# Optimization experiments

Hardware: AMD Instinct MI355X
Metric: run time of the kernel (lower is better)

## Reference

```python
import jax, jax.numpy as jnp
import numpy as np

EPS = 1e-5
NH, NP = 4, 4  # num_heads, num_points (num_levels = 1)


def layer_norm(x, g, b):
    m = jnp.mean(x, -1, keepdims=True)
    xc = x - m
    v = jnp.mean(xc * xc, -1, keepdims=True)
    return xc * jax.lax.rsqrt(v + EPS) * g + b


def setup_inputs() -> dict:
    key = jax.random.key(0)
    ks = jax.random.split(key, 8)
    B, C, H, W = 8, 256, 64, 64
    s = 0.02
    return {
        "x1": jax.random.normal(ks[0], (B, C, H, W), jnp.float32),
        "x2": jax.random.normal(ks[1], (B, C, H, W), jnp.float32),
        "ln1_g": jnp.ones((C,), jnp.float32),
        "ln1_b": jnp.zeros((C,), jnp.float32),
        "ln2_g": jnp.ones((C,), jnp.float32),
        "ln2_b": jnp.zeros((C,), jnp.float32),
        "pos_scale": jnp.ones((1,), jnp.float32),
        "W_off": jax.random.normal(ks[2], (C, NH * NP * 2), jnp.float32) * s,
        "b_off": jax.random.normal(ks[3], (NH * NP * 2,), jnp.float32) * 0.5,
        "W_att": jax.random.normal(ks[4], (C, NH * NP), jnp.float32) * s,
        "b_att": jnp.zeros((NH * NP,), jnp.float32),
        "W_val": jax.random.normal(ks[5], (C, C), jnp.float32) * s,
        "b_val": jnp.zeros((C,), jnp.float32),
        "W_out": jax.random.normal(ks[6], (C, C), jnp.float32) * s,
        "b_out": jnp.zeros((C,), jnp.float32),
    }


def reference(x1, x2, ln1_g, ln1_b, ln2_g, ln2_b, pos_scale,
              W_off, b_off, W_att, b_att, W_val, b_val, W_out, b_out):
    B, C, H, W = x1.shape
    Nq = H * W
    d = C // NH
    q_in = x1.reshape(B, C, Nq).transpose(0, 2, 1)   # (B, Nq, C)
    v_in = x2.reshape(B, C, Nq).transpose(0, 2, 1)   # (B, Nv, C), identity

    # ScaledSinuEmbedding positional encoding over the query sequence
    inv_freq = 1.0 / (10000.0 ** (jnp.arange(0, C, 2, dtype=jnp.float32) / C))
    sinu = jnp.arange(Nq, dtype=jnp.float32)[:, None] * inv_freq[None, :]
    qpos = jnp.concatenate([jnp.sin(sinu), jnp.cos(sinu)], -1) * pos_scale  # (Nq, C)

    query = layer_norm(q_in, ln1_g, ln1_b) + qpos[None]
    value = layer_norm(v_in, ln2_g, ln2_b) @ W_val + b_val                 # (B, Nv, C)
    value = value.reshape(B, Nq, NH, d).transpose(0, 2, 1, 3)              # (B, NH, Nv, d)

    off = (query @ W_off + b_off).reshape(B, Nq, NH, NP, 2)
    att = jax.nn.softmax((query @ W_att + b_att).reshape(B, Nq, NH, NP), axis=-1)

    # reference points: normalized pixel centers of the query grid
    ry, rx = jnp.meshgrid((jnp.arange(H, dtype=jnp.float32) + 0.5) / H,
                          (jnp.arange(W, dtype=jnp.float32) + 0.5) / W,
                          indexing="ij")
    ref = jnp.stack([rx.ravel(), ry.ravel()], -1)                          # (Nq, 2) as (x, y)

    norm = jnp.array([W, H], jnp.float32)  # offset_normalizer = (W, H)
    loc = ref[None, :, None, None, :] + off / norm                         # (B,Nq,NH,NP,2)
    loc = loc.transpose(0, 2, 1, 3, 4)                                     # (B,NH,Nq,NP,2)
    # grid_sample(align_corners=False): pixel = normalized * size - 0.5
    px = loc[..., 0] * W - 0.5
    py = loc[..., 1] * H - 0.5
    x0 = jnp.floor(px); y0 = jnp.floor(py)
    wx = px - x0; wy = py - y0
    x0i = x0.astype(jnp.int32); y0i = y0.astype(jnp.int32)

    def gather(ix, iy):
        # zero padding for out-of-bounds corners, like grid_sample(padding_mode='zeros')
        valid = ((ix >= 0) & (ix < W) & (iy >= 0) & (iy < H)).astype(value.dtype)
        idx = jnp.clip(iy, 0, H - 1) * W + jnp.clip(ix, 0, W - 1)          # (B,NH,Nq,NP)
        g = jnp.take_along_axis(value, idx.reshape(B, NH, Nq * NP, 1), axis=2)
        return g.reshape(B, NH, Nq, NP, d) * valid[..., None]

    sampled = (gather(x0i, y0i) * ((1 - wx) * (1 - wy))[..., None]
               + gather(x0i + 1, y0i) * (wx * (1 - wy))[..., None]
               + gather(x0i, y0i + 1) * ((1 - wx) * wy)[..., None]
               + gather(x0i + 1, y0i + 1) * (wx * wy)[..., None])          # (B,NH,Nq,NP,d)

    out = jnp.sum(sampled * att.transpose(0, 2, 1, 3)[..., None], axis=3)  # (B,NH,Nq,d)
    out = out.transpose(0, 2, 1, 3).reshape(B, Nq, C)
    out = out @ W_out + b_out + v_in                                       # + identity (x2)
    return out.transpose(0, 2, 1).reshape(B, C, H, W)
```

## Files before the change

kernel.cpp:

```cpp
#include <hip/hip_runtime.h>
#include <math.h>

namespace {
constexpr int kC = 256;
constexpr int kNq = 4096;
constexpr int kM = 32768;
}

typedef __attribute__((ext_vector_type(8))) short short8;
typedef __attribute__((ext_vector_type(4))) float f32x4;

__device__ inline unsigned short f2bf(float f) {
  union { float f; unsigned u; } v; v.f = f;
  unsigned r = (v.u + 0x7FFFu + ((v.u >> 16) & 1u)) >> 16;
  return (unsigned short)r;
}
__device__ inline float uasf(unsigned u) {
  union { unsigned u; float f; } v; v.u = u; return v.f;
}

__global__ __launch_bounds__(256)
void prep_weights_kernel(const float* __restrict__ Wv, const float* __restrict__ Wo,
                         const float* __restrict__ Woff, const float* __restrict__ Watt,
                         unsigned short* __restrict__ WvT, unsigned short* __restrict__ WoT,
                         unsigned short* __restrict__ WoaT) {
  const int i = blockIdx.x * 256 + threadIdx.x;
  {
    const int n = i >> 8, k = i & 255;
    WvT[i] = f2bf(Wv[k * 256 + n]);
    WoT[i] = f2bf(Wo[k * 256 + n]);
  }
  if (i < 16384) {
    const int j = i >> 8, k = i & 255;
    float v = 0.f;
    if (j < 32) v = Woff[k * 32 + j];
    else if (j < 48) v = Watt[k * 16 + (j - 32)];
    WoaT[i] = f2bf(v);
  }
}


__global__ __launch_bounds__(256)
void fused_val_kernel(const float* __restrict__ X, const float* __restrict__ gam,
                      const float* __restrict__ beta, const unsigned short* __restrict__ Wt,
                      const float* __restrict__ bias, unsigned short* __restrict__ V) {
  __shared__ unsigned short As[64][264];
  __shared__ float scratch[256][33];
  __shared__ float psum[8][32];
  __shared__ float psq[8][32];
  __shared__ float smean[64];
  __shared__ float srstd[64];

  const int m0 = blockIdx.x * 64;
  const int b = m0 >> 12;
  const int n0 = m0 & 4095;
  const int tid = threadIdx.x;
  const float gc = gam[tid];
  const float bc = beta[tid];
  const float* Xb = X + (size_t)b * kC * kNq;

  for (int grp = 0; grp < 2; ++grp) {
    float4 vbuf[8];
#pragma unroll
    for (int it = 0; it < 8; ++it) {
      const int i = it * 256 + tid;
      const int c = i >> 3, q4 = (i & 7) * 4;
      vbuf[it] = *(const float4*)&Xb[(size_t)c * kNq + n0 + grp * 32 + q4];
    }
#pragma unroll
    for (int it = 0; it < 8; ++it) {
      const int i = it * 256 + tid;
      const int c = i >> 3, q4 = (i & 7) * 4;
      scratch[c][q4 + 0] = vbuf[it].x;
      scratch[c][q4 + 1] = vbuf[it].y;
      scratch[c][q4 + 2] = vbuf[it].z;
      scratch[c][q4 + 3] = vbuf[it].w;
    }
    __syncthreads();
    {
      const int nn = tid & 31, cg = tid >> 5;
      float s = 0.f, sq = 0.f;
#pragma unroll
      for (int cc = 0; cc < 32; ++cc) {
        const float v = scratch[cg * 32 + cc][nn];
        s += v; sq += v * v;
      }
      psum[cg][nn] = s; psq[cg][nn] = sq;
    }
    __syncthreads();
    if (tid < 32) {
      float S = 0.f, Q = 0.f;
#pragma unroll
      for (int g = 0; g < 8; ++g) { S += psum[g][tid]; Q += psq[g][tid]; }
      const float m = S * (1.f / 256.f);
      const float v = Q * (1.f / 256.f) - m * m;
      smean[grp * 32 + tid] = m;
      srstd[grp * 32 + tid] = rsqrtf(v + 1e-5f);
    }
    __syncthreads();
    for (int q = 0; q < 32; ++q) {
      const int row = grp * 32 + q;
      As[row][tid] = f2bf((scratch[tid][q] - smean[row]) * srstd[row] * gc + bc);
    }
    __syncthreads();
  }

  const int lane = tid & 63, w = tid >> 6;
  const int l15 = lane & 15, quad = lane >> 4;
  f32x4 acc[4][4];
#pragma unroll
  for (int i = 0; i < 4; ++i)
#pragma unroll
    for (int j = 0; j < 4; ++j) acc[i][j] = (f32x4){0.f, 0.f, 0.f, 0.f};

#pragma unroll
  for (int s = 0; s < 8; ++s) {
    short8 af[4], wf[4];
#pragma unroll
    for (int t = 0; t < 4; ++t) af[t] = *(const short8*)&As[t * 16 + l15][s * 32 + quad * 8];
#pragma unroll
    for (int t = 0; t < 4; ++t)
      wf[t] = *(const short8*)&Wt[(size_t)(w * 64 + t * 16 + l15) * 256 + s * 32 + quad * 8];
#pragma unroll
    for (int i = 0; i < 4; ++i)
#pragma unroll
      for (int j = 0; j < 4; ++j)
        acc[i][j] = __builtin_amdgcn_mfma_f32_16x16x32_bf16(af[i], wf[j], acc[i][j], 0, 0, 0);
  }
#pragma unroll
  for (int i = 0; i < 4; ++i)
#pragma unroll
    for (int j = 0; j < 4; ++j) {
      const int n = w * 64 + j * 16 + l15;
      const float bn = bias[n];
#pragma unroll
      for (int r = 0; r < 4; ++r) {
        const int m = m0 + i * 16 + quad * 4 + r;
        V[(size_t)m * 256 + n] = f2bf(acc[i][j][r] + bn);
      }
    }
}

__global__ __launch_bounds__(256)
void fused_offatt_kernel(const float* __restrict__ X, const float* __restrict__ gam,
                         const float* __restrict__ beta, const float* __restrict__ ps,
                         const unsigned short* __restrict__ Wt,
                         const float* __restrict__ boff, const float* __restrict__ batt,
                         float* __restrict__ RAW) {
  __shared__ unsigned short As[64][264];
  __shared__ float scratch[256][33];
  __shared__ float psum[8][32];
  __shared__ float psq[8][32];
  __shared__ float smean[64];
  __shared__ float srstd[64];

  const int m0 = blockIdx.x * 64;
  const int b = m0 >> 12;
  const int n0 = m0 & 4095;
  const int tid = threadIdx.x;
  const float gc = gam[tid];
  const float bc = beta[tid];
  const float scale = ps[0];
  const int i2 = (tid < 128) ? tid : (tid - 128);
  const float invf = powf(10000.f, -(float)(2 * i2) * (1.f / 256.f));
  const float* Xb = X + (size_t)b * kC * kNq;

  for (int grp = 0; grp < 2; ++grp) {
    float4 vbuf[8];
#pragma unroll
    for (int it = 0; it < 8; ++it) {
      const int i = it * 256 + tid;
      const int c = i >> 3, q4 = (i & 7) * 4;
      vbuf[it] = *(const float4*)&Xb[(size_t)c * kNq + n0 + grp * 32 + q4];
    }
#pragma unroll
    for (int it = 0; it < 8; ++it) {
      const int i = it * 256 + tid;
      const int c = i >> 3, q4 = (i & 7) * 4;
      scratch[c][q4 + 0] = vbuf[it].x;
      scratch[c][q4 + 1] = vbuf[it].y;
      scratch[c][q4 + 2] = vbuf[it].z;
      scratch[c][q4 + 3] = vbuf[it].w;
    }
    __syncthreads();
    {
      const int nn = tid & 31, cg = tid >> 5;
      float s = 0.f, sq = 0.f;
#pragma unroll
      for (int cc = 0; cc < 32; ++cc) {
        const float v = scratch[cg * 32 + cc][nn];
        s += v; sq += v * v;
      }
      psum[cg][nn] = s; psq[cg][nn] = sq;
    }
    __syncthreads();
    if (tid < 32) {
      float S = 0.f, Q = 0.f;
#pragma unroll
      for (int g = 0; g < 8; ++g) { S += psum[g][tid]; Q += psq[g][tid]; }
      const float m = S * (1.f / 256.f);
      const float v = Q * (1.f / 256.f) - m * m;
      smean[grp * 32 + tid] = m;
      srstd[grp * 32 + tid] = rsqrtf(v + 1e-5f);
    }
    __syncthreads();
    for (int q = 0; q < 32; ++q) {
      const int row = grp * 32 + q;
      float val = (scratch[tid][q] - smean[row]) * srstd[row] * gc + bc;
      const float a = (float)(n0 + row) * invf;
      val += ((tid < 128) ? sinf(a) : cosf(a)) * scale;
      As[row][tid] = f2bf(val);
    }
    __syncthreads();
  }

  const int lane = tid & 63, w = tid >> 6;
  const int l15 = lane & 15, quad = lane >> 4;
  f32x4 acc[3];
#pragma unroll
  for (int j = 0; j < 3; ++j) acc[j] = (f32x4){0.f, 0.f, 0.f, 0.f};
#pragma unroll
  for (int s = 0; s < 8; ++s) {
    short8 af = *(const short8*)&As[w * 16 + l15][s * 32 + quad * 8];
    short8 wf[3];
#pragma unroll
    for (int t = 0; t < 3; ++t)
      wf[t] = *(const short8*)&Wt[(size_t)(t * 16 + l15) * 256 + s * 32 + quad * 8];
#pragma unroll
    for (int j = 0; j < 3; ++j)
      acc[j] = __builtin_amdgcn_mfma_f32_16x16x32_bf16(af, wf[j], acc[j], 0, 0, 0);
  }
#pragma unroll
  for (int j = 0; j < 3; ++j) {
    const int n = j * 16 + l15;
    const float bn = (n < 32) ? boff[n] : batt[n - 32];
#pragma unroll
    for (int r = 0; r < 4; ++r) {
      const int m = m0 + w * 16 + quad * 4 + r;
      RAW[(size_t)m * 48 + n] = acc[j][r] + bn;
    }
  }
}

__global__ __launch_bounds__(256)
void sample_kernel(const float* __restrict__ RAW, const unsigned short* __restrict__ V,
                   unsigned short* __restrict__ AO) {
  __shared__ int sidx[128][4];
  __shared__ float swgt[128][4];
  const int blk = blockIdx.x;
  const int m0 = ((blk & 7) * 512 + (blk >> 3)) * 8;
  const int b = m0 >> 12;
  const int tid = threadIdx.x;

  if (tid < 128) {
    const int q_l = tid >> 4, h = (tid >> 2) & 3, p = tid & 3;
    const int m = m0 + q_l;
    const float* raw = RAW + (size_t)m * 48;
    const float l0 = raw[32 + h * 4 + 0];
    const float l1 = raw[32 + h * 4 + 1];
    const float l2 = raw[32 + h * 4 + 2];
    const float l3 = raw[32 + h * 4 + 3];
    const float mx = fmaxf(fmaxf(l0, l1), fmaxf(l2, l3));
    const float e0 = expf(l0 - mx), e1 = expf(l1 - mx), e2 = expf(l2 - mx), e3 = expf(l3 - mx);
    const float lp = (p == 0) ? e0 : (p == 1) ? e1 : (p == 2) ? e2 : e3;
    const float attp = lp / (e0 + e1 + e2 + e3);

    const float ox = raw[h * 8 + p * 2 + 0];
    const float oy = raw[h * 8 + p * 2 + 1];
    const float px = (float)(m & 63) + ox;
    const float py = (float)((m >> 6) & 63) + oy;
    const float fx = floorf(px), fy = floorf(py);
    const float wx = px - fx, wy = py - fy;
    const int x0 = (int)fx, y0 = (int)fy;
#pragma unroll
    for (int c = 0; c < 4; ++c) {
      const int dx = c & 1, dy = c >> 1;
      const int xx = x0 + dx, yy = y0 + dy;
      const bool valid = (xx >= 0) & (xx < 64) & (yy >= 0) & (yy < 64);
      const float wc = (dx ? wx : 1.f - wx) * (dy ? wy : 1.f - wy) * attp;
      swgt[tid][c] = valid ? wc : 0.f;
      const int xc = min(max(xx, 0), 63), yc = min(max(yy, 0), 63);
      sidx[tid][c] = yc * 64 + xc;
    }
  }
  __syncthreads();

  const int q_l = tid >> 5, sub = tid & 31;
  const int h = sub >> 3, c8 = (sub & 7) * 8;
  const int trip0 = q_l * 16 + h * 4;
  const unsigned short* vb = V + (size_t)b * kNq * kC + h * 64 + c8;
  float acc[8] = {};
#pragma unroll
  for (int p = 0; p < 4; ++p) {
    const int4 idx = *(const int4*)&sidx[trip0 + p][0];
    const float4 wv = *(const float4*)&swgt[trip0 + p][0];
    const int ia[4] = {idx.x, idx.y, idx.z, idx.w};
    const float wa[4] = {wv.x, wv.y, wv.z, wv.w};
#pragma unroll
    for (int c = 0; c < 4; ++c) {
      const uint4 u = *(const uint4*)&vb[(size_t)ia[c] * kC];
      const float w = wa[c];
      acc[0] = fmaf(w, uasf(u.x << 16), acc[0]);
      acc[1] = fmaf(w, uasf(u.x & 0xffff0000u), acc[1]);
      acc[2] = fmaf(w, uasf(u.y << 16), acc[2]);
      acc[3] = fmaf(w, uasf(u.y & 0xffff0000u), acc[3]);
      acc[4] = fmaf(w, uasf(u.z << 16), acc[4]);
      acc[5] = fmaf(w, uasf(u.z & 0xffff0000u), acc[5]);
      acc[6] = fmaf(w, uasf(u.w << 16), acc[6]);
      acc[7] = fmaf(w, uasf(u.w & 0xffff0000u), acc[7]);
    }
  }
  const int m = m0 + q_l;
  short8 outv;
#pragma unroll
  for (int e = 0; e < 8; ++e) outv[e] = (short)f2bf(acc[e]);
  *(short8*)&AO[(size_t)m * kC + h * 64 + c8] = outv;
}

__global__ __launch_bounds__(256, 3)
void gemm_out_kernel(const unsigned short* __restrict__ Wt,
                     const unsigned short* __restrict__ AO,
                     const float* __restrict__ bias, const float* __restrict__ x2,
                     float* __restrict__ OUT) {
  __shared__ unsigned short Bs[64][264];
  const int q0 = blockIdx.x * 64;
  const int tid = threadIdx.x;
  const int lane = tid & 63, w = tid >> 6;
  const int l15 = lane & 15, quad = lane >> 4;

#pragma unroll
  for (int it = 0; it < 8; ++it) {
    const int i = it * 256 + tid;
    const int r = i >> 5, cc = (i & 31) * 8;
    *(short8*)&Bs[r][cc] = *(const short8*)&AO[(size_t)(q0 + r) * 256 + cc];
  }
  __syncthreads();

  f32x4 acc[4][4];
#pragma unroll
  for (int i = 0; i < 4; ++i)
#pragma unroll
    for (int j = 0; j < 4; ++j) acc[i][j] = (f32x4){0.f, 0.f, 0.f, 0.f};

#pragma unroll
  for (int s = 0; s < 8; ++s) {
    short8 wf[4], bf[4];
#pragma unroll
    for (int t = 0; t < 4; ++t)
      wf[t] = *(const short8*)&Wt[(size_t)(w * 64 + t * 16 + l15) * 256 + s * 32 + quad * 8];
#pragma unroll
    for (int t = 0; t < 4; ++t) bf[t] = *(const short8*)&Bs[t * 16 + l15][s * 32 + quad * 8];
#pragma unroll
    for (int i = 0; i < 4; ++i)
#pragma unroll
      for (int j = 0; j < 4; ++j)
        acc[i][j] = __builtin_amdgcn_mfma_f32_16x16x32_bf16(wf[i], bf[j], acc[i][j], 0, 0, 0);
  }

  const int b = q0 >> 12;
  const int qb = q0 & 4095;
#pragma unroll
  for (int i = 0; i < 4; ++i) {
#pragma unroll
    for (int r = 0; r < 4; ++r) {
      const int c = w * 64 + i * 16 + quad * 4 + r;
      const float bc = bias[c];
      const size_t rowbase = ((size_t)b * 256 + c) * 4096 + qb;
#pragma unroll
      for (int j = 0; j < 4; ++j) {
        const int q = j * 16 + l15;
        OUT[rowbase + q] = acc[i][j][r] + bc + x2[rowbase + q];
      }
    }
  }
}

extern "C" void kernel_launch(void* const* d_in, const int* in_sizes, int n_in,
                              void* d_out, int out_size, void* d_ws, size_t ws_size,
                              hipStream_t stream) {
  const float* x1 = (const float*)d_in[0];
  const float* x2 = (const float*)d_in[1];
  const float* ln1_g = (const float*)d_in[2];
  const float* ln1_b = (const float*)d_in[3];
  const float* ln2_g = (const float*)d_in[4];
  const float* ln2_b = (const float*)d_in[5];
  const float* pos_scale = (const float*)d_in[6];
  const float* W_off = (const float*)d_in[7];
  const float* b_off = (const float*)d_in[8];
  const float* W_att = (const float*)d_in[9];
  const float* b_att = (const float*)d_in[10];
  const float* W_val = (const float*)d_in[11];
  const float* b_val = (const float*)d_in[12];
  const float* W_out = (const float*)d_in[13];
  const float* b_out = (const float*)d_in[14];
  float* out = (float*)d_out;

  char* ws = (char*)d_ws;
  const size_t plane2 = (size_t)kM * kC * sizeof(unsigned short);
  unsigned short* Vb   = (unsigned short*)(ws);
  unsigned short* AOb  = (unsigned short*)(ws + plane2);
  float* RAW           = (float*)(ws + 2 * plane2);
  unsigned short* WvT  = (unsigned short*)(ws + 2 * plane2 + (size_t)kM * 48 * 4);
  unsigned short* WoT  = WvT + 65536;
  unsigned short* WoaT = WoT + 65536;

  prep_weights_kernel<<<256, 256, 0, stream>>>(W_val, W_out, W_off, W_att, WvT, WoT, WoaT);
  fused_offatt_kernel<<<kM / 64, 256, 0, stream>>>(x1, ln1_g, ln1_b, pos_scale, WoaT,
                                                   b_off, b_att, RAW);
  fused_val_kernel<<<kM / 64, 256, 0, stream>>>(x2, ln2_g, ln2_b, WvT, b_val, Vb);
  sample_kernel<<<kM / 8, 256, 0, stream>>>(RAW, Vb, AOb);
  gemm_out_kernel<<<kM / 64, 256, 0, stream>>>(WoT, AOb, b_out, x2, out);
}
```

Baseline: 201.6 us.

## Merge LN-GEMM kernels and fuse sampling with output projection

Result: faster. 185.0 us (-8.2%).

```diff
diff --git a/kernel.cpp b/kernel.cpp
--- a/kernel.cpp
+++ b/kernel.cpp
@@ -39,11 +39,16 @@
   }
 }
 
-
 __global__ __launch_bounds__(256)
-void fused_val_kernel(const float* __restrict__ X, const float* __restrict__ gam,
-                      const float* __restrict__ beta, const unsigned short* __restrict__ Wt,
-                      const float* __restrict__ bias, unsigned short* __restrict__ V) {
+void fused_ln_gemm_kernel(const float* __restrict__ x1, const float* __restrict__ x2,
+                          const float* __restrict__ ln1_g, const float* __restrict__ ln1_b,
+                          const float* __restrict__ ln2_g, const float* __restrict__ ln2_b,
+                          const float* __restrict__ ps,
+                          const unsigned short* __restrict__ WvT,
+                          const float* __restrict__ b_val, unsigned short* __restrict__ V,
+                          const unsigned short* __restrict__ WoaT,
+                          const float* __restrict__ boff, const float* __restrict__ batt,
+                          float* __restrict__ RAW) {
   __shared__ unsigned short As[64][264];
   __shared__ float scratch[256][33];
   __shared__ float psum[8][32];
@@ -51,12 +56,20 @@
   __shared__ float smean[64];
   __shared__ float srstd[64];
 
-  const int m0 = blockIdx.x * 64;
+  const int mode = blockIdx.x & 1;
+  const int m0 = (blockIdx.x >> 1) * 64;
   const int b = m0 >> 12;
   const int n0 = m0 & 4095;
   const int tid = threadIdx.x;
-  const float gc = gam[tid];
-  const float bc = beta[tid];
+  const float* X = mode ? x1 : x2;
+  const float gc = mode ? ln1_g[tid] : ln2_g[tid];
+  const float bc = mode ? ln1_b[tid] : ln2_b[tid];
+  float scale = 0.f, invf = 0.f;
+  if (mode) {
+    scale = ps[0];
+    const int i2 = (tid < 128) ? tid : (tid - 128);
+    invf = powf(10000.f, -(float)(2 * i2) * (1.f / 256.f));
+  }
   const float* Xb = X + (size_t)b * kC * kNq;
 
   for (int grp = 0; grp < 2; ++grp) {
@@ -98,162 +111,107 @@
       srstd[grp * 32 + tid] = rsqrtf(v + 1e-5f);
     }
     __syncthreads();
-    for (int q = 0; q < 32; ++q) {
-      const int row = grp * 32 + q;
-      As[row][tid] = f2bf((scratch[tid][q] - smean[row]) * srstd[row] * gc + bc);
+    if (mode) {
+      for (int q = 0; q < 32; ++q) {
+        const int row = grp * 32 + q;
+        float val = (scratch[tid][q] - smean[row]) * srstd[row] * gc + bc;
+        const float a = (float)(n0 + row) * invf;
+        val += ((tid < 128) ? sinf(a) : cosf(a)) * scale;
+        As[row][tid] = f2bf(val);
+      }
+    } else {
+      for (int q = 0; q < 32; ++q) {
+        const int row = grp * 32 + q;
+        As[row][tid] = f2bf((scratch[tid][q] - smean[row]) * srstd[row] * gc + bc);
+      }
     }
     __syncthreads();
   }
 
   const int lane = tid & 63, w = tid >> 6;
   const int l15 = lane & 15, quad = lane >> 4;
-  f32x4 acc[4][4];
-#pragma unroll
-  for (int i = 0; i < 4; ++i)
-#pragma unroll
-    for (int j = 0; j < 4; ++j) acc[i][j] = (f32x4){0.f, 0.f, 0.f, 0.f};
-
-#pragma unroll
-  for (int s = 0; s < 8; ++s) {
-    short8 af[4], wf[4];
-#pragma unroll
-    for (int t = 0; t < 4; ++t) af[t] = *(const short8*)&As[t * 16 + l15][s * 32 + quad * 8];
-#pragma unroll
-    for (int t = 0; t < 4; ++t)
-      wf[t] = *(const short8*)&Wt[(size_t)(w * 64 + t * 16 + l15) * 256 + s * 32 + quad * 8];
+
+  if (mode == 0) {
+    f32x4 acc[4][4];
 #pragma unroll
     for (int i = 0; i < 4; ++i)
 #pragma unroll
-      for (int j = 0; j < 4; ++j)
-        acc[i][j] = __builtin_amdgcn_mfma_f32_16x16x32_bf16(af[i], wf[j], acc[i][j], 0, 0, 0);
-  }
-#pragma unroll
-  for (int i = 0; i < 4; ++i)
-#pragma unroll
-    for (int j = 0; j < 4; ++j) {
-      const int n = w * 64 + j * 16 + l15;
-      const float bn = bias[n];
+      for (int j = 0; j < 4; ++j) acc[i][j] = (f32x4){0.f, 0.f, 0.f, 0.f};
+#pragma unroll
+    for (int s = 0; s < 8; ++s) {
+      short8 af[4], wf[4];
+#pragma unroll
+      for (int t = 0; t < 4; ++t) af[t] = *(const short8*)&As[t * 16 + l15][s * 32 + quad * 8];
+#pragma unroll
+      for (int t = 0; t < 4; ++t)
+        wf[t] = *(const short8*)&WvT[(size_t)(w * 64 + t * 16 + l15) * 256 + s * 32 + quad * 8];
+#pragma unroll
+      for (int i = 0; i < 4; ++i)
+#pragma unroll
+        for (int j = 0; j < 4; ++j)
+          acc[i][j] = __builtin_amdgcn_mfma_f32_16x16x32_bf16(af[i], wf[j], acc[i][j], 0, 0, 0);
+    }
+#pragma unroll
+    for (int i = 0; i < 4; ++i)
+#pragma unroll
+      for (int j = 0; j < 4; ++j) {
+        const int n = w * 64 + j * 16 + l15;
+        const float bn = b_val[n];
+#pragma unroll
+        for (int r = 0; r < 4; ++r) {
+          const int m = m0 + i * 16 + quad * 4 + r;
+          V[(size_t)m * 256 + n] = f2bf(acc[i][j][r] + bn);
+        }
+      }
+  } else {
+    f32x4 acc[3];
+#pragma unroll
+    for (int j = 0; j < 3; ++j) acc[j] = (f32x4){0.f, 0.f, 0.f, 0.f};
+#pragma unroll
+    for (int s = 0; s < 8; ++s) {
+      short8 af = *(const short8*)&As[w * 16 + l15][s * 32 + quad * 8];
+      short8 wf[3];
+#pragma unroll
+      for (int t = 0; t < 3; ++t)
+        wf[t] = *(const short8*)&WoaT[(size_t)(t * 16 + l15) * 256 + s * 32 + quad * 8];
+#pragma unroll
+      for (int j = 0; j < 3; ++j)
+        acc[j] = __builtin_amdgcn_mfma_f32_16x16x32_bf16(af, wf[j], acc[j], 0, 0, 0);
+    }
+#pragma unroll
+    for (int j = 0; j < 3; ++j) {
+      const int n = j * 16 + l15;
+      const float bn = (n < 32) ? boff[n] : batt[n - 32];
 #pragma unroll
       for (int r = 0; r < 4; ++r) {
-        const int m = m0 + i * 16 + quad * 4 + r;
-        V[(size_t)m * 256 + n] = f2bf(acc[i][j][r] + bn);
-      }
-    }
+        const int m = m0 + w * 16 + quad * 4 + r;
+        RAW[(size_t)m * 48 + n] = acc[j][r] + bn;
+      }
+    }
+  }
 }
 
 __global__ __launch_bounds__(256)
-void fused_offatt_kernel(const float* __restrict__ X, const float* __restrict__ gam,
-                         const float* __restrict__ beta, const float* __restrict__ ps,
-                         const unsigned short* __restrict__ Wt,
-                         const float* __restrict__ boff, const float* __restrict__ batt,
-                         float* __restrict__ RAW) {
-  __shared__ unsigned short As[64][264];
-  __shared__ float scratch[256][33];
-  __shared__ float psum[8][32];
-  __shared__ float psq[8][32];
-  __shared__ float smean[64];
-  __shared__ float srstd[64];
-
-  const int m0 = blockIdx.x * 64;
-  const int b = m0 >> 12;
-  const int n0 = m0 & 4095;
+void sample_out_kernel(const float* __restrict__ RAW, const unsigned short* __restrict__ V,
+                       const unsigned short* __restrict__ Wt,
+                       const float* __restrict__ bias, const float* __restrict__ x2,
+                       float* __restrict__ OUT) {
+  __shared__ unsigned short Bs[64][264];
+  __shared__ __align__(16) char smemA[32768];
+  int (*sidx)[4] = (int(*)[4])smemA;
+  float (*swgt)[4] = (float(*)[4])(smemA + 16384);
+  float* ot = (float*)smemA;
+
+  const int blk = blockIdx.x;
+  const int b = blk & 7;
+  const int tile = blk >> 3;
+  const int m0 = b * 4096 + tile * 64;
   const int tid = threadIdx.x;
-  const float gc = gam[tid];
-  const float bc = beta[tid];
-  const float scale = ps[0];
-  const int i2 = (tid < 128) ? tid : (tid - 128);
-  const float invf = powf(10000.f, -(float)(2 * i2) * (1.f / 256.f));
-  const float* Xb = X + (size_t)b * kC * kNq;
-
-  for (int grp = 0; grp < 2; ++grp) {
-    float4 vbuf[8];
-#pragma unroll
-    for (int it = 0; it < 8; ++it) {
-      const int i = it * 256 + tid;
-      const int c = i >> 3, q4 = (i & 7) * 4;
-      vbuf[it] = *(const float4*)&Xb[(size_t)c * kNq + n0 + grp * 32 + q4];
-    }
-#pragma unroll
-    for (int it = 0; it < 8; ++it) {
-      const int i = it * 256 + tid;
-      const int c = i >> 3, q4 = (i & 7) * 4;
-      scratch[c][q4 + 0] = vbuf[it].x;
-      scratch[c][q4 + 1] = vbuf[it].y;
-      scratch[c][q4 + 2] = vbuf[it].z;
-      scratch[c][q4 + 3] = vbuf[it].w;
-    }
-    __syncthreads();
-    {
-      const int nn = tid & 31, cg = tid >> 5;
-      float s = 0.f, sq = 0.f;
-#pragma unroll
-      for (int cc = 0; cc < 32; ++cc) {
-        const float v = scratch[cg * 32 + cc][nn];
-        s += v; sq += v * v;
-      }
-      psum[cg][nn] = s; psq[cg][nn] = sq;
-    }
-    __syncthreads();
-    if (tid < 32) {
-      float S = 0.f, Q = 0.f;
-#pragma unroll
-      for (int g = 0; g < 8; ++g) { S += psum[g][tid]; Q += psq[g][tid]; }
-      const float m = S * (1.f / 256.f);
-      const float v = Q * (1.f / 256.f) - m * m;
-      smean[grp * 32 + tid] = m;
-      srstd[grp * 32 + tid] = rsqrtf(v + 1e-5f);
-    }
-    __syncthreads();
-    for (int q = 0; q < 32; ++q) {
-      const int row = grp * 32 + q;
-      float val = (scratch[tid][q] - smean[row]) * srstd[row] * gc + bc;
-      const float a = (float)(n0 + row) * invf;
-      val += ((tid < 128) ? sinf(a) : cosf(a)) * scale;
-      As[row][tid] = f2bf(val);
-    }
-    __syncthreads();
-  }
-
-  const int lane = tid & 63, w = tid >> 6;
-  const int l15 = lane & 15, quad = lane >> 4;
-  f32x4 acc[3];
-#pragma unroll
-  for (int j = 0; j < 3; ++j) acc[j] = (f32x4){0.f, 0.f, 0.f, 0.f};
-#pragma unroll
-  for (int s = 0; s < 8; ++s) {
-    short8 af = *(const short8*)&As[w * 16 + l15][s * 32 + quad * 8];
-    short8 wf[3];
-#pragma unroll
-    for (int t = 0; t < 3; ++t)
-      wf[t] = *(const short8*)&Wt[(size_t)(t * 16 + l15) * 256 + s * 32 + quad * 8];
-#pragma unroll
-    for (int j = 0; j < 3; ++j)
-      acc[j] = __builtin_amdgcn_mfma_f32_16x16x32_bf16(af, wf[j], acc[j], 0, 0, 0);
-  }
-#pragma unroll
-  for (int j = 0; j < 3; ++j) {
-    const int n = j * 16 + l15;
-    const float bn = (n < 32) ? boff[n] : batt[n - 32];
-#pragma unroll
-    for (int r = 0; r < 4; ++r) {
-      const int m = m0 + w * 16 + quad * 4 + r;
-      RAW[(size_t)m * 48 + n] = acc[j][r] + bn;
-    }
-  }
-}
-
-__global__ __launch_bounds__(256)
-void sample_kernel(const float* __restrict__ RAW, const unsigned short* __restrict__ V,
-                   unsigned short* __restrict__ AO) {
-  __shared__ int sidx[128][4];
-  __shared__ float swgt[128][4];
-  const int blk = blockIdx.x;
-  const int m0 = ((blk & 7) * 512 + (blk >> 3)) * 8;
-  const int b = m0 >> 12;
-  const int tid = threadIdx.x;
-
-  if (tid < 128) {
-    const int q_l = tid >> 4, h = (tid >> 2) & 3, p = tid & 3;
+
+#pragma unroll
+  for (int t = 0; t < 4; ++t) {
+    const int trip = t * 256 + tid;
+    const int q_l = trip >> 4, h = (trip >> 2) & 3, p = trip & 3;
     const int m = m0 + q_l;
     const float* raw = RAW + (size_t)m * 48;
     const float l0 = raw[32 + h * 4 + 0];
@@ -278,70 +236,55 @@
       const int xx = x0 + dx, yy = y0 + dy;
       const bool valid = (xx >= 0) & (xx < 64) & (yy >= 0) & (yy < 64);
       const float wc = (dx ? wx : 1.f - wx) * (dy ? wy : 1.f - wy) * attp;
-      swgt[tid][c] = valid ? wc : 0.f;
+      swgt[trip][c] = valid ? wc : 0.f;
       const int xc = min(max(xx, 0), 63), yc = min(max(yy, 0), 63);
-      sidx[tid][c] = yc * 64 + xc;
+      sidx[trip][c] = yc * 64 + xc;
     }
   }
   __syncthreads();
 
-  const int q_l = tid >> 5, sub = tid & 31;
-  const int h = sub >> 3, c8 = (sub & 7) * 8;
-  const int trip0 = q_l * 16 + h * 4;
-  const unsigned short* vb = V + (size_t)b * kNq * kC + h * 64 + c8;
-  float acc[8] = {};
-#pragma unroll
-  for (int p = 0; p < 4; ++p) {
-    const int4 idx = *(const int4*)&sidx[trip0 + p][0];
-    const float4 wv = *(const float4*)&swgt[trip0 + p][0];
-    const int ia[4] = {idx.x, idx.y, idx.z, idx.w};
-    const float wa[4] = {wv.x, wv.y, wv.z, wv.w};
-#pragma unroll
-    for (int c = 0; c < 4; ++c) {
-      const uint4 u = *(const uint4*)&vb[(size_t)ia[c] * kC];
-      const float w = wa[c];
-      acc[0] = fmaf(w, uasf(u.x << 16), acc[0]);
-      acc[1] = fmaf(w, uasf(u.x & 0xffff0000u), acc[1]);
-      acc[2] = fmaf(w, uasf(u.y << 16), acc[2]);
-      acc[3] = fmaf(w, uasf(u.y & 0xffff0000u), acc[3]);
-      acc[4] = fmaf(w, uasf(u.z << 16), acc[4]);
-      acc[5] = fmaf(w, uasf(u.z & 0xffff0000u), acc[5]);
-      acc[6] = fmaf(w, uasf(u.w << 16), acc[6]);
-      acc[7] = fmaf(w, uasf(u.w & 0xffff0000u), acc[7]);
-    }
-  }
-  const int m = m0 + q_l;
-  short8 outv;
-#pragma unroll
-  for (int e = 0; e < 8; ++e) outv[e] = (short)f2bf(acc[e]);
-  *(short8*)&AO[(size_t)m * kC + h * 64 + c8] = outv;
-}
-
-__global__ __launch_bounds__(256, 3)
-void gemm_out_kernel(const unsigned short* __restrict__ Wt,
-                     const unsigned short* __restrict__ AO,
-                     const float* __restrict__ bias, const float* __restrict__ x2,
-                     float* __restrict__ OUT) {
-  __shared__ unsigned short Bs[64][264];
-  const int q0 = blockIdx.x * 64;
-  const int tid = threadIdx.x;
+#pragma unroll
+  for (int it = 0; it < 8; ++it) {
+    const int lin = it * 256 + tid;
+    const int q_l = lin >> 5, sub = lin & 31;
+    const int h = sub >> 3, c8 = (sub & 7) * 8;
+    const int trip0 = q_l * 16 + h * 4;
+    const unsigned short* vb = V + (size_t)b * kNq * kC + h * 64 + c8;
+    float acc[8] = {};
+#pragma unroll
+    for (int p = 0; p < 4; ++p) {
+      const int4 idx = *(const int4*)&sidx[trip0 + p][0];
+      const float4 wv = *(const float4*)&swgt[trip0 + p][0];
+      const int ia[4] = {idx.x, idx.y, idx.z, idx.w};
+      const float wa[4] = {wv.x, wv.y, wv.z, wv.w};
+#pragma unroll
+      for (int c = 0; c < 4; ++c) {
+        const uint4 u = *(const uint4*)&vb[(size_t)ia[c] * kC];
+        const float w = wa[c];
+        acc[0] = fmaf(w, uasf(u.x << 16), acc[0]);
+        acc[1] = fmaf(w, uasf(u.x & 0xffff0000u), acc[1]);
+        acc[2] = fmaf(w, uasf(u.y << 16), acc[2]);
+        acc[3] = fmaf(w, uasf(u.y & 0xffff0000u), acc[3]);
+        acc[4] = fmaf(w, uasf(u.z << 16), acc[4]);
+        acc[5] = fmaf(w, uasf(u.z & 0xffff0000u), acc[5]);
+        acc[6] = fmaf(w, uasf(u.w << 16), acc[6]);
+        acc[7] = fmaf(w, uasf(u.w & 0xffff0000u), acc[7]);
+      }
+    }
+    short8 outv;
+#pragma unroll
+    for (int e = 0; e < 8; ++e) outv[e] = (short)f2bf(acc[e]);
+    *(short8*)&Bs[q_l][h * 64 + c8] = outv;
+  }
+  __syncthreads();
+
   const int lane = tid & 63, w = tid >> 6;
   const int l15 = lane & 15, quad = lane >> 4;
-
-#pragma unroll
-  for (int it = 0; it < 8; ++it) {
-    const int i = it * 256 + tid;
-    const int r = i >> 5, cc = (i & 31) * 8;
-    *(short8*)&Bs[r][cc] = *(const short8*)&AO[(size_t)(q0 + r) * 256 + cc];
-  }
-  __syncthreads();
-
   f32x4 acc[4][4];
 #pragma unroll
   for (int i = 0; i < 4; ++i)
 #pragma unroll
     for (int j = 0; j < 4; ++j) acc[i][j] = (f32x4){0.f, 0.f, 0.f, 0.f};
-
 #pragma unroll
   for (int s = 0; s < 8; ++s) {
     short8 wf[4], bf[4];
@@ -357,20 +300,34 @@
         acc[i][j] = __builtin_amdgcn_mfma_f32_16x16x32_bf16(wf[i], bf[j], acc[i][j], 0, 0, 0);
   }
 
-  const int b = q0 >> 12;
-  const int qb = q0 & 4095;
-#pragma unroll
-  for (int i = 0; i < 4; ++i) {
-#pragma unroll
-    for (int r = 0; r < 4; ++r) {
-      const int c = w * 64 + i * 16 + quad * 4 + r;
+  const int whalf = w >> 1;
+  const int clbase = (w & 1) * 64;
+  for (int ch = 0; ch < 2; ++ch) {
+    __syncthreads();
+    if (whalf == ch) {
+#pragma unroll
+      for (int i = 0; i < 4; ++i)
+#pragma unroll
+        for (int j = 0; j < 4; ++j)
+#pragma unroll
+          for (int r = 0; r < 4; ++r)
+            ot[(clbase + i * 16 + quad * 4 + r) * 64 + j * 16 + l15] = acc[i][j][r];
+    }
+    __syncthreads();
+#pragma unroll
+    for (int t = 0; t < 8; ++t) {
+      const int lin = t * 256 + tid;
+      const int cl = lin >> 4, q4 = (lin & 15) * 4;
+      const int c = ch * 128 + cl;
+      const size_t rowbase = ((size_t)b * 256 + c) * 4096 + tile * 64;
+      const float4 xv = *(const float4*)&x2[rowbase + q4];
       const float bc = bias[c];
-      const size_t rowbase = ((size_t)b * 256 + c) * 4096 + qb;
-#pragma unroll
-      for (int j = 0; j < 4; ++j) {
-        const int q = j * 16 + l15;
-        OUT[rowbase + q] = acc[i][j][r] + bc + x2[rowbase + q];
-      }
+      float4 o;
+      o.x = ot[cl * 64 + q4 + 0] + bc + xv.x;
+      o.y = ot[cl * 64 + q4 + 1] + bc + xv.y;
+      o.z = ot[cl * 64 + q4 + 2] + bc + xv.z;
+      o.w = ot[cl * 64 + q4 + 3] + bc + xv.w;
+      *(float4*)&OUT[rowbase + q4] = o;
     }
   }
 }
@@ -398,16 +355,14 @@
   char* ws = (char*)d_ws;
   const size_t plane2 = (size_t)kM * kC * sizeof(unsigned short);
   unsigned short* Vb   = (unsigned short*)(ws);
-  unsigned short* AOb  = (unsigned short*)(ws + plane2);
-  float* RAW           = (float*)(ws + 2 * plane2);
-  unsigned short* WvT  = (unsigned short*)(ws + 2 * plane2 + (size_t)kM * 48 * 4);
+  float* RAW           = (float*)(ws + plane2);
+  unsigned short* WvT  = (unsigned short*)(ws + plane2 + (size_t)kM * 48 * 4);
   unsigned short* WoT  = WvT + 65536;
   unsigned short* WoaT = WoT + 65536;
 
   prep_weights_kernel<<<256, 256, 0, stream>>>(W_val, W_out, W_off, W_att, WvT, WoT, WoaT);
-  fused_offatt_kernel<<<kM / 64, 256, 0, stream>>>(x1, ln1_g, ln1_b, pos_scale, WoaT,
-                                                   b_off, b_att, RAW);
-  fused_val_kernel<<<kM / 64, 256, 0, stream>>>(x2, ln2_g, ln2_b, WvT, b_val, Vb);
-  sample_kernel<<<kM / 8, 256, 0, stream>>>(RAW, Vb, AOb);
-  gemm_out_kernel<<<kM / 64, 256, 0, stream>>>(WoT, AOb, b_out, x2, out);
-}
+  fused_ln_gemm_kernel<<<1024, 256, 0, stream>>>(x1, x2, ln1_g, ln1_b, ln2_g, ln2_b,
+                                                 pos_scale, WvT, b_val, Vb,
+                                                 WoaT, b_off, b_att, RAW);
+  sample_out_kernel<<<512, 256, 0, stream>>>(RAW, Vb, WoT, b_out, x2, out);
+}
```
